# Performance work log

Hardware: AMD Instinct MI355X
Metric: run time of the kernel (lower is better)

## Reference

```python
import jax, jax.numpy as jnp
import numpy as np

HIDDEN = 1024
NUM_HEADS = 16
HEAD_DIM = HIDDEN // NUM_HEADS
SCALE = HEAD_DIM ** -0.5
BATCH = 32
T_CACHED = 2047


def setup_inputs() -> dict:
    key = jax.random.key(0)
    ks = jax.random.split(key, 8)
    hidden_states = jax.random.normal(ks[0], (BATCH, 1, HIDDEN), dtype=jnp.float32)
    key_cache = jax.random.normal(ks[1], (BATCH, NUM_HEADS, T_CACHED, HEAD_DIM), dtype=jnp.float32)
    value_cache = jax.random.normal(ks[2], (BATCH, NUM_HEADS, T_CACHED, HEAD_DIM), dtype=jnp.float32)
    block_tables = jax.random.randint(ks[3], (BATCH, 128), 0, 1024, dtype=jnp.int64 if jax.config.jax_enable_x64 else jnp.int32)
    # valid lengths in [1, T_cached+1]
    seq_lens = jax.random.randint(ks[4], (BATCH,), 1, T_CACHED + 2, dtype=jnp.int32)
    W_attn = jax.random.normal(ks[5], (HIDDEN, 3 * HIDDEN), dtype=jnp.float32) * (HIDDEN ** -0.5)
    b_attn = jnp.zeros((3 * HIDDEN,), dtype=jnp.float32)
    W_proj = jax.random.normal(ks[6], (HIDDEN, HIDDEN), dtype=jnp.float32) * (HIDDEN ** -0.5)
    b_proj = jnp.zeros((HIDDEN,), dtype=jnp.float32)
    return {
        "hidden_states": hidden_states,
        "key_cache": key_cache,
        "value_cache": value_cache,
        "block_tables": block_tables,
        "seq_lens": seq_lens,
        "max_seq_len": T_CACHED + 1,
        "W_attn": W_attn,
        "b_attn": b_attn,
        "W_proj": W_proj,
        "b_proj": b_proj,
    }


def reference(hidden_states, key_cache, value_cache, block_tables, seq_lens,
              max_seq_len, W_attn, b_attn, W_proj, b_proj):
    B, S, H = hidden_states.shape  # S == 1 (single-query decode)
    hs = hidden_states.reshape(B, H)
    qkv = hs @ W_attn + b_attn                      # [B, 3H]
    q, k, v = jnp.split(qkv, 3, axis=-1)
    q = q.reshape(B, NUM_HEADS, HEAD_DIM)           # [B, h, d]
    k = k.reshape(B, NUM_HEADS, 1, HEAD_DIM)
    v = v.reshape(B, NUM_HEADS, 1, HEAD_DIM)
    K = jnp.concatenate([key_cache, k], axis=2)     # [B, h, T, d]
    V = jnp.concatenate([value_cache, v], axis=2)
    T = K.shape[2]
    # single-query attention: scores [B, h, T]
    scores = jnp.einsum('bhd,bhtd->bht', q, K) * SCALE
    pos = jnp.arange(T)
    # attend to first seq_len cached tokens; the freshly appended token (pos T-1) is always visible
    valid = (pos[None, :] < seq_lens[:, None]) | (pos[None, :] == T - 1)  # [B, T]
    scores = jnp.where(valid[:, None, :], scores, jnp.float32(-1e30))
    p = jax.nn.softmax(scores, axis=-1)
    out = jnp.einsum('bht,bhtd->bhd', p, V)         # [B, h, d]
    attn_output = out.reshape(B, S, H) @ W_proj + b_proj
    return attn_output, K, V
```

## Files before the change

### kernel.cpp

```cpp
#include <hip/hip_runtime.h>
#include <math.h>

#define BATCH   32
#define NH      16
#define HD      64
#define T_ALL   2048
#define T_CACHE 2047
#define HID     1024
#define H3      3072
#define QK_SCALE 0.125f
#define NCHUNK  16
#define CHTOK   128
#define NWIN    8
#define KSPLIT  8

typedef float f4 __attribute__((ext_vector_type(4)));

template<int NB>
__global__ __launch_bounds__(256) void gemv_part_kernel(
    const float* __restrict__ X, const float* __restrict__ W,
    float* __restrict__ part, int N, int Kdim)
{
    const int c  = blockIdx.x * 256 + threadIdx.x;
    const int ks = blockIdx.y;
    const int b0 = blockIdx.z * NB;
    const int kchunk = Kdim / KSPLIT;
    float acc[NB];
#pragma unroll
    for (int j = 0; j < NB; ++j) acc[j] = 0.f;
    const int k0 = ks * kchunk;
#pragma unroll 16
    for (int k = k0; k < k0 + kchunk; ++k) {
        const float w = W[(size_t)k * N + c];
#pragma unroll
        for (int j = 0; j < NB; ++j)
            acc[j] = fmaf(X[(b0 + j) * Kdim + k], w, acc[j]);
    }
#pragma unroll
    for (int j = 0; j < NB; ++j)
        part[((size_t)ks * BATCH + b0 + j) * N + c] = acc[j];
}

__global__ __launch_bounds__(256) void gemv_reduce_kernel(
    const float* __restrict__ part, const float* __restrict__ bias,
    float* __restrict__ out, int N)
{
    const int c4 = blockIdx.x * 256 + threadIdx.x;
    const int b  = blockIdx.y;
    const int N4 = N >> 2;
    f4 acc = ((const f4*)bias)[c4];
#pragma unroll
    for (int ks = 0; ks < KSPLIT; ++ks) {
        const f4 p = ((const f4*)part)[((size_t)ks * BATCH + b) * N4 + c4];
        acc.x += p.x; acc.y += p.y; acc.z += p.z; acc.w += p.w;
    }
    ((f4*)out)[(size_t)b * N4 + c4] = acc;
}

__global__ __launch_bounds__(256, 4) void fused_copy_attn_kernel(
    const float* __restrict__ kc, const float* __restrict__ vc,
    const float* __restrict__ qkv, const int* __restrict__ seq_lens,
    float* __restrict__ Kout, float* __restrict__ Vout,
    float* __restrict__ Pm, float* __restrict__ Pl, float* __restrict__ Po)
{
    const int chunk = blockIdx.x;
    const int h     = blockIdx.y;
    const int b     = blockIdx.z;
    const int tid   = threadIdx.x;
    const int wave  = tid >> 6;
    const int lane  = tid & 63;
    const int dgrp  = lane & 15;
    const int tgrp  = lane >> 4;

    const int bh   = b * NH + h;
    const int slen = seq_lens[b];

    const f4 q4 = ((const f4*)(qkv + (size_t)b * H3 + h * HD))[dgrp];

    const int t0 = chunk * CHTOK + wave * (NWIN * 4);
    const int tl = t0 + tgrp;
    const int nat  = min(NWIN, max(0, (slen - t0 + 3) >> 2));
    const bool tail = (t0 + NWIN * 4 - 1 >= T_CACHE);

    const f4* kbase = (const f4*)(kc + (size_t)bh * T_CACHE * HD) + (size_t)tl * 16 + dgrp;
    const f4* vbase = (const f4*)(vc + (size_t)bh * T_CACHE * HD) + (size_t)tl * 16 + dgrp;
    f4* Kb = (f4*)(Kout + (size_t)bh * T_ALL * HD) + (size_t)tl * 16 + dgrp;
    f4* Vb = (f4*)(Vout + (size_t)bh * T_ALL * HD) + (size_t)tl * 16 + dgrp;

    f4 kreg[NWIN], vreg[NWIN];
    float s[NWIN];

    if (!tail) {
#pragma unroll
        for (int i = 0; i < NWIN; ++i)
            kreg[i] = __builtin_nontemporal_load(kbase + i * 64);
#pragma unroll
        for (int i = 0; i < NWIN; ++i)
            vreg[i] = __builtin_nontemporal_load(vbase + i * 64);

#pragma unroll
        for (int i = 0; i < NWIN; ++i) {
            __builtin_nontemporal_store(kreg[i], Kb + i * 64);
            if (i < nat) {
                const f4 kv = kreg[i];
                float ss = kv.x * q4.x + kv.y * q4.y + kv.z * q4.z + kv.w * q4.w;
                ss += __shfl_xor(ss, 1);
                ss += __shfl_xor(ss, 2);
                ss += __shfl_xor(ss, 4);
                ss += __shfl_xor(ss, 8);
                s[i] = (tl + i * 4 < slen) ? ss * QK_SCALE : -1e30f;
            }
        }
    } else {
#pragma unroll
        for (int i = 0; i < NWIN; ++i) {
            const int t = tl + i * 4;
            kreg[i] = (f4){0.f, 0.f, 0.f, 0.f};
            vreg[i] = (f4){0.f, 0.f, 0.f, 0.f};
            if (t < T_CACHE) {
                kreg[i] = __builtin_nontemporal_load(kbase + i * 64);
                vreg[i] = __builtin_nontemporal_load(vbase + i * 64);
            }
        }
#pragma unroll
        for (int i = 0; i < NWIN; ++i) {
            const int t = tl + i * 4;
            if (t < T_CACHE)
                __builtin_nontemporal_store(kreg[i], Kb + i * 64);
            if (i < nat) {
                const f4 kv = kreg[i];
                float ss = kv.x * q4.x + kv.y * q4.y + kv.z * q4.z + kv.w * q4.w;
                ss += __shfl_xor(ss, 1);
                ss += __shfl_xor(ss, 2);
                ss += __shfl_xor(ss, 4);
                ss += __shfl_xor(ss, 8);
                s[i] = (t < slen && t < T_CACHE) ? ss * QK_SCALE : -1e30f;
            }
        }
    }

    float m = -1e30f;
#pragma unroll
    for (int i = 0; i < NWIN; ++i)
        if (i < nat) m = fmaxf(m, s[i]);
    m = fmaxf(m, __shfl_xor(m, 16));
    m = fmaxf(m, __shfl_xor(m, 32));

    float l = 0.f;
#pragma unroll
    for (int i = 0; i < NWIN; ++i)
        if (i < nat) {
            const float p = __expf(s[i] - m);
            s[i] = p;
            l += p;
        }

    f4 o = {0.f, 0.f, 0.f, 0.f};
    if (!tail) {
#pragma unroll
        for (int i = 0; i < NWIN; ++i) {
            __builtin_nontemporal_store(vreg[i], Vb + i * 64);
            if (i < nat) {
                o.x = fmaf(s[i], vreg[i].x, o.x);
                o.y = fmaf(s[i], vreg[i].y, o.y);
                o.z = fmaf(s[i], vreg[i].z, o.z);
                o.w = fmaf(s[i], vreg[i].w, o.w);
            }
        }
    } else {
#pragma unroll
        for (int i = 0; i < NWIN; ++i) {
            const int t = tl + i * 4;
            if (t < T_CACHE)
                __builtin_nontemporal_store(vreg[i], Vb + i * 64);
            if (i < nat) {
                o.x = fmaf(s[i], vreg[i].x, o.x);
                o.y = fmaf(s[i], vreg[i].y, o.y);
                o.z = fmaf(s[i], vreg[i].z, o.z);
                o.w = fmaf(s[i], vreg[i].w, o.w);
            }
        }
    }

    l += __shfl_xor(l, 16); l += __shfl_xor(l, 32);
    o.x += __shfl_xor(o.x, 16); o.x += __shfl_xor(o.x, 32);
    o.y += __shfl_xor(o.y, 16); o.y += __shfl_xor(o.y, 32);
    o.z += __shfl_xor(o.z, 16); o.z += __shfl_xor(o.z, 32);
    o.w += __shfl_xor(o.w, 16); o.w += __shfl_xor(o.w, 32);

    __shared__ float sm[4], sl[4];
    __shared__ f4 so4[4][16];
    if (lane == 0) { sm[wave] = m; sl[wave] = l; }
    if (lane < 16) so4[wave][dgrp] = o;
    __syncthreads();

    if (tid < HD) {
        const int d = tid;
        const float m0 = sm[0], m1 = sm[1], m2 = sm[2], m3 = sm[3];
        const float mc = fmaxf(fmaxf(m0, m1), fmaxf(m2, m3));
        const float e0 = __expf(m0 - mc), e1 = __expf(m1 - mc);
        const float e2 = __expf(m2 - mc), e3 = __expf(m3 - mc);
        const float lc = sl[0]*e0 + sl[1]*e1 + sl[2]*e2 + sl[3]*e3;
        const float* so = (const float*)so4;
        const float oc = so[0*HD + d]*e0 + so[1*HD + d]*e1
                       + so[2*HD + d]*e2 + so[3*HD + d]*e3;
        const int pb = bh * NCHUNK + chunk;
        Po[(size_t)pb * HD + d] = oc;
        if (d == 0) { Pm[pb] = mc; Pl[pb] = lc; }
    }
}

__global__ __launch_bounds__(64) void combine_kernel(
    const float* __restrict__ qkv,
    const float* __restrict__ Pm, const float* __restrict__ Pl,
    const float* __restrict__ Po,
    float* __restrict__ attn, float* __restrict__ Kout, float* __restrict__ Vout)
{
    const int bh = blockIdx.x;
    const int b = bh >> 4, h = bh & 15;
    const int d = threadIdx.x;

    const float* qb = qkv + (size_t)b * H3;
    const float qd = qb[h * HD + d];
    const float kn = qb[HID  + h * HD + d];
    const float vn = qb[2*HID + h * HD + d];

    Kout[((size_t)bh * T_ALL + (T_ALL - 1)) * HD + d] = kn;
    Vout[((size_t)bh * T_ALL + (T_ALL - 1)) * HD + d] = vn;

    float s = qd * kn;
    s += __shfl_xor(s, 1);
    s += __shfl_xor(s, 2);
    s += __shfl_xor(s, 4);
    s += __shfl_xor(s, 8);
    s += __shfl_xor(s, 16);
    s += __shfl_xor(s, 32);
    s *= QK_SCALE;

    float mg = s;
#pragma unroll
    for (int c = 0; c < NCHUNK; ++c)
        mg = fmaxf(mg, Pm[bh * NCHUNK + c]);

    float L   = __expf(s - mg);
    float acc = L * vn;
#pragma unroll
    for (int c = 0; c < NCHUNK; ++c) {
        const float e = __expf(Pm[bh * NCHUNK + c] - mg);
        acc += Po[(size_t)(bh * NCHUNK + c) * HD + d] * e;
        L   += Pl[bh * NCHUNK + c] * e;
    }
    attn[(size_t)b * HID + h * HD + d] = acc / L;
}

extern "C" void kernel_launch(void* const* d_in, const int* in_sizes, int n_in,
                              void* d_out, int out_size, void* d_ws, size_t ws_size,
                              hipStream_t stream)
{
    const float* hs       = (const float*)d_in[0];
    const float* kc       = (const float*)d_in[1];
    const float* vc       = (const float*)d_in[2];
    const int*   seq_lens = (const int*)d_in[4];
    const float* W_attn   = (const float*)d_in[6];
    const float* b_attn   = (const float*)d_in[7];
    const float* W_proj   = (const float*)d_in[8];
    const float* b_proj   = (const float*)d_in[9];

    float* out_attn = (float*)d_out;
    float* Kout = out_attn + (size_t)BATCH * HID;
    float* Vout = Kout + (size_t)BATCH * NH * T_ALL * HD;

    float* w = (float*)d_ws;
    float* w_qkv_part  = w;
    float* w_qkv       = w_qkv_part + (size_t)KSPLIT * BATCH * H3;
    float* w_Pm        = w_qkv + (size_t)BATCH * H3;
    float* w_Pl        = w_Pm + BATCH * NH * NCHUNK;
    float* w_Po        = w_Pl + BATCH * NH * NCHUNK;
    float* w_attnvec   = w_Po + (size_t)BATCH * NH * NCHUNK * HD;
    float* w_proj_part = w_attnvec + (size_t)BATCH * HID;

    gemv_part_kernel<16><<<dim3(H3 / 256, KSPLIT, 2), 256, 0, stream>>>(
        hs, W_attn, w_qkv_part, H3, HID);
    gemv_reduce_kernel<<<dim3(H3 / 4 / 256, BATCH), 256, 0, stream>>>(
        w_qkv_part, b_attn, w_qkv, H3);

    fused_copy_attn_kernel<<<dim3(NCHUNK, NH, BATCH), 256, 0, stream>>>(
        kc, vc, w_qkv, seq_lens, Kout, Vout, w_Pm, w_Pl, w_Po);

    combine_kernel<<<dim3(BATCH * NH), 64, 0, stream>>>(
        w_qkv, w_Pm, w_Pl, w_Po, w_attnvec, Kout, Vout);

    gemv_part_kernel<8><<<dim3(HID / 256, KSPLIT, 4), 256, 0, stream>>>(
        w_attnvec, W_proj, w_proj_part, HID, HID);
    gemv_reduce_kernel<<<dim3(HID / 4 / 256, BATCH), 256, 0, stream>>>(
        w_proj_part, b_proj, out_attn, HID);
}
```

Measured before the change: 251.3 us.

## Fuse QKV split-K reduction into attention and combine; halve chunk size

Removes the separate QKV reduce kernel launch. The attention and combine kernels now sum the split-K partials plus bias themselves, which costs a few redundant loads per block. It also doubles the number of attention chunks (64 tokens each, 4 windows per wave) and raises the occupancy hint to 6 blocks per CU, aiming for more parallelism and lower register pressure. The trade-off is a larger combine step and more partial-result traffic.

```diff
diff --git a/kernel.cpp b/kernel.cpp
--- a/kernel.cpp
+++ b/kernel.cpp
@@ -9,9 +9,9 @@
 #define HID     1024
 #define H3      3072
 #define QK_SCALE 0.125f
-#define NCHUNK  16
-#define CHTOK   128
-#define NWIN    8
+#define NCHUNK  32
+#define CHTOK   64
+#define NWIN    4
 #define KSPLIT  8
 
 typedef float f4 __attribute__((ext_vector_type(4)));
@@ -57,9 +57,10 @@
     ((f4*)out)[(size_t)b * N4 + c4] = acc;
 }
 
-__global__ __launch_bounds__(256, 4) void fused_copy_attn_kernel(
+__global__ __launch_bounds__(256, 6) void fused_copy_attn_kernel(
     const float* __restrict__ kc, const float* __restrict__ vc,
-    const float* __restrict__ qkv, const int* __restrict__ seq_lens,
+    const float* __restrict__ qkv_part, const float* __restrict__ b_attn,
+    const int* __restrict__ seq_lens,
     float* __restrict__ Kout, float* __restrict__ Vout,
     float* __restrict__ Pm, float* __restrict__ Pl, float* __restrict__ Po)
 {
@@ -75,7 +76,12 @@
     const int bh   = b * NH + h;
     const int slen = seq_lens[b];
 
-    const f4 q4 = ((const f4*)(qkv + (size_t)b * H3 + h * HD))[dgrp];
+    f4 q4 = ((const f4*)(b_attn + h * HD))[dgrp];
+#pragma unroll
+    for (int ks = 0; ks < KSPLIT; ++ks) {
+        const f4 p = ((const f4*)(qkv_part + ((size_t)ks * BATCH + b) * H3 + h * HD))[dgrp];
+        q4.x += p.x; q4.y += p.y; q4.z += p.z; q4.w += p.w;
+    }
 
     const int t0 = chunk * CHTOK + wave * (NWIN * 4);
     const int tl = t0 + tgrp;
@@ -211,7 +217,7 @@
 }
 
 __global__ __launch_bounds__(64) void combine_kernel(
-    const float* __restrict__ qkv,
+    const float* __restrict__ qkv_part, const float* __restrict__ b_attn,
     const float* __restrict__ Pm, const float* __restrict__ Pl,
     const float* __restrict__ Po,
     float* __restrict__ attn, float* __restrict__ Kout, float* __restrict__ Vout)
@@ -220,10 +226,16 @@
     const int b = bh >> 4, h = bh & 15;
     const int d = threadIdx.x;
 
-    const float* qb = qkv + (size_t)b * H3;
-    const float qd = qb[h * HD + d];
-    const float kn = qb[HID  + h * HD + d];
-    const float vn = qb[2*HID + h * HD + d];
+    float qd = b_attn[h * HD + d];
+    float kn = b_attn[HID  + h * HD + d];
+    float vn = b_attn[2*HID + h * HD + d];
+#pragma unroll
+    for (int ks = 0; ks < KSPLIT; ++ks) {
+        const float* pp = qkv_part + ((size_t)ks * BATCH + b) * H3;
+        qd += pp[h * HD + d];
+        kn += pp[HID  + h * HD + d];
+        vn += pp[2*HID + h * HD + d];
+    }
 
     Kout[((size_t)bh * T_ALL + (T_ALL - 1)) * HD + d] = kn;
     Vout[((size_t)bh * T_ALL + (T_ALL - 1)) * HD + d] = vn;
@@ -238,13 +250,13 @@
     s *= QK_SCALE;
 
     float mg = s;
-#pragma unroll
+#pragma unroll 16
     for (int c = 0; c < NCHUNK; ++c)
         mg = fmaxf(mg, Pm[bh * NCHUNK + c]);
 
     float L   = __expf(s - mg);
     float acc = L * vn;
-#pragma unroll
+#pragma unroll 8
     for (int c = 0; c < NCHUNK; ++c) {
         const float e = __expf(Pm[bh * NCHUNK + c] - mg);
         acc += Po[(size_t)(bh * NCHUNK + c) * HD + d] * e;
@@ -272,8 +284,7 @@
 
     float* w = (float*)d_ws;
     float* w_qkv_part  = w;
-    float* w_qkv       = w_qkv_part + (size_t)KSPLIT * BATCH * H3;
-    float* w_Pm        = w_qkv + (size_t)BATCH * H3;
+    float* w_Pm        = w_qkv_part + (size_t)KSPLIT * BATCH * H3;
     float* w_Pl        = w_Pm + BATCH * NH * NCHUNK;
     float* w_Po        = w_Pl + BATCH * NH * NCHUNK;
     float* w_attnvec   = w_Po + (size_t)BATCH * NH * NCHUNK * HD;
@@ -281,14 +292,12 @@
 
     gemv_part_kernel<16><<<dim3(H3 / 256, KSPLIT, 2), 256, 0, stream>>>(
         hs, W_attn, w_qkv_part, H3, HID);
-    gemv_reduce_kernel<<<dim3(H3 / 4 / 256, BATCH), 256, 0, stream>>>(
-        w_qkv_part, b_attn, w_qkv, H3);
 
     fused_copy_attn_kernel<<<dim3(NCHUNK, NH, BATCH), 256, 0, stream>>>(
-        kc, vc, w_qkv, seq_lens, Kout, Vout, w_Pm, w_Pl, w_Po);
+        kc, vc, w_qkv_part, b_attn, seq_lens, Kout, Vout, w_Pm, w_Pl, w_Po);
 
     combine_kernel<<<dim3(BATCH * NH), 64, 0, stream>>>(
-        w_qkv, w_Pm, w_Pl, w_Po, w_attnvec, Kout, Vout);
+        w_qkv_part, b_attn, w_Pm, w_Pl, w_Po, w_attnvec, Kout, Vout);
 
     gemv_part_kernel<8><<<dim3(HID / 256, KSPLIT, 4), 256, 0, stream>>>(
         w_attnvec, W_proj, w_proj_part, HID, HID);
```

New measurement: 243.0 us (median of 2 runs). 1.03x faster.

## Split fused K/V copy-attention into separate K-score and V-accumulate kernels

Applied to the files above, without the earlier changes.

The single kernel that copied K and V while computing chunked attention becomes two kernels. The first copies K, computes scores and the chunk-max-normalised probabilities, and writes them to workspace. The second copies V and accumulates the probability-weighted output. The aim is to halve register pressure per kernel (occupancy hint raised from 4 to 6) so more loads are in flight, at the cost of an extra launch and a round trip of the probabilities through global memory. The workspace is also reorganised so several scratch buffers share one region.

```diff
diff --git a/kernel.cpp b/kernel.cpp
--- a/kernel.cpp
+++ b/kernel.cpp
@@ -57,11 +57,11 @@
     ((f4*)out)[(size_t)b * N4 + c4] = acc;
 }
 
-__global__ __launch_bounds__(256, 4) void fused_copy_attn_kernel(
-    const float* __restrict__ kc, const float* __restrict__ vc,
-    const float* __restrict__ qkv, const int* __restrict__ seq_lens,
-    float* __restrict__ Kout, float* __restrict__ Vout,
-    float* __restrict__ Pm, float* __restrict__ Pl, float* __restrict__ Po)
+__global__ __launch_bounds__(256, 6) void k_copy_score_kernel(
+    const float* __restrict__ kc, const float* __restrict__ qkv,
+    const int* __restrict__ seq_lens,
+    float* __restrict__ Kout,
+    float* __restrict__ Pm, float* __restrict__ Pl, float* __restrict__ P)
 {
     const int chunk = blockIdx.x;
     const int h     = blockIdx.y;
@@ -73,21 +73,19 @@
     const int tgrp  = lane >> 4;
 
     const int bh   = b * NH + h;
-    const int slen = seq_lens[b];
+    const int vlim = min(seq_lens[b], T_CACHE);
 
     const f4 q4 = ((const f4*)(qkv + (size_t)b * H3 + h * HD))[dgrp];
 
     const int t0 = chunk * CHTOK + wave * (NWIN * 4);
     const int tl = t0 + tgrp;
-    const int nat  = min(NWIN, max(0, (slen - t0 + 3) >> 2));
+    const int nat  = min(NWIN, max(0, (vlim - t0 + 3) >> 2));
     const bool tail = (t0 + NWIN * 4 - 1 >= T_CACHE);
 
     const f4* kbase = (const f4*)(kc + (size_t)bh * T_CACHE * HD) + (size_t)tl * 16 + dgrp;
-    const f4* vbase = (const f4*)(vc + (size_t)bh * T_CACHE * HD) + (size_t)tl * 16 + dgrp;
     f4* Kb = (f4*)(Kout + (size_t)bh * T_ALL * HD) + (size_t)tl * 16 + dgrp;
-    f4* Vb = (f4*)(Vout + (size_t)bh * T_ALL * HD) + (size_t)tl * 16 + dgrp;
-
-    f4 kreg[NWIN], vreg[NWIN];
+
+    f4 kreg[NWIN];
     float s[NWIN];
 
     if (!tail) {
@@ -95,47 +93,38 @@
         for (int i = 0; i < NWIN; ++i)
             kreg[i] = __builtin_nontemporal_load(kbase + i * 64);
 #pragma unroll
-        for (int i = 0; i < NWIN; ++i)
-            vreg[i] = __builtin_nontemporal_load(vbase + i * 64);
-
-#pragma unroll
         for (int i = 0; i < NWIN; ++i) {
             __builtin_nontemporal_store(kreg[i], Kb + i * 64);
-            if (i < nat) {
-                const f4 kv = kreg[i];
-                float ss = kv.x * q4.x + kv.y * q4.y + kv.z * q4.z + kv.w * q4.w;
-                ss += __shfl_xor(ss, 1);
-                ss += __shfl_xor(ss, 2);
-                ss += __shfl_xor(ss, 4);
-                ss += __shfl_xor(ss, 8);
-                s[i] = (tl + i * 4 < slen) ? ss * QK_SCALE : -1e30f;
-            }
+            s[i] = kreg[i].x * q4.x + kreg[i].y * q4.y
+                 + kreg[i].z * q4.z + kreg[i].w * q4.w;
         }
     } else {
 #pragma unroll
         for (int i = 0; i < NWIN; ++i) {
             const int t = tl + i * 4;
             kreg[i] = (f4){0.f, 0.f, 0.f, 0.f};
-            vreg[i] = (f4){0.f, 0.f, 0.f, 0.f};
-            if (t < T_CACHE) {
+            if (t < T_CACHE)
                 kreg[i] = __builtin_nontemporal_load(kbase + i * 64);
-                vreg[i] = __builtin_nontemporal_load(vbase + i * 64);
-            }
         }
 #pragma unroll
         for (int i = 0; i < NWIN; ++i) {
             const int t = tl + i * 4;
             if (t < T_CACHE)
                 __builtin_nontemporal_store(kreg[i], Kb + i * 64);
-            if (i < nat) {
-                const f4 kv = kreg[i];
-                float ss = kv.x * q4.x + kv.y * q4.y + kv.z * q4.z + kv.w * q4.w;
-                ss += __shfl_xor(ss, 1);
-                ss += __shfl_xor(ss, 2);
-                ss += __shfl_xor(ss, 4);
-                ss += __shfl_xor(ss, 8);
-                s[i] = (t < slen && t < T_CACHE) ? ss * QK_SCALE : -1e30f;
-            }
+            s[i] = kreg[i].x * q4.x + kreg[i].y * q4.y
+                 + kreg[i].z * q4.z + kreg[i].w * q4.w;
+        }
+    }
+
+#pragma unroll
+    for (int i = 0; i < NWIN; ++i) {
+        if (i < nat) {
+            float ss = s[i];
+            ss += __shfl_xor(ss, 1);
+            ss += __shfl_xor(ss, 2);
+            ss += __shfl_xor(ss, 4);
+            ss += __shfl_xor(ss, 8);
+            s[i] = (tl + i * 4 < vlim) ? ss * QK_SCALE : -1e30f;
         }
     }
 
@@ -146,26 +135,95 @@
     m = fmaxf(m, __shfl_xor(m, 16));
     m = fmaxf(m, __shfl_xor(m, 32));
 
+    __shared__ float sm[4], sl[4];
+    if (lane == 0) sm[wave] = m;
+    __syncthreads();
+    const float mc = fmaxf(fmaxf(sm[0], sm[1]), fmaxf(sm[2], sm[3]));
+
     float l = 0.f;
 #pragma unroll
     for (int i = 0; i < NWIN; ++i)
         if (i < nat) {
-            const float p = __expf(s[i] - m);
+            const float p = __expf(s[i] - mc);
             s[i] = p;
             l += p;
         }
+    l += __shfl_xor(l, 16); l += __shfl_xor(l, 32);
+
+    const int pb = bh * NCHUNK + chunk;
+    if (dgrp == 0) {
+#pragma unroll
+        for (int i = 0; i < NWIN; ++i)
+            if (i < nat)
+                P[(size_t)pb * CHTOK + wave * (NWIN * 4) + i * 4 + tgrp] = s[i];
+    }
+    if (lane == 0) sl[wave] = l;
+    __syncthreads();
+    if (tid == 0) {
+        Pm[pb] = mc;
+        Pl[pb] = sl[0] + sl[1] + sl[2] + sl[3];
+    }
+}
+
+__global__ __launch_bounds__(256, 6) void v_copy_accum_kernel(
+    const float* __restrict__ vc, const int* __restrict__ seq_lens,
+    const float* __restrict__ P,
+    float* __restrict__ Vout, float* __restrict__ Po)
+{
+    const int chunk = blockIdx.x;
+    const int h     = blockIdx.y;
+    const int b     = blockIdx.z;
+    const int tid   = threadIdx.x;
+    const int wave  = tid >> 6;
+    const int lane  = tid & 63;
+    const int dgrp  = lane & 15;
+    const int tgrp  = lane >> 4;
+
+    const int bh   = b * NH + h;
+    const int vlim = min(seq_lens[b], T_CACHE);
+
+    const int t0 = chunk * CHTOK + wave * (NWIN * 4);
+    const int tl = t0 + tgrp;
+    const int nat  = min(NWIN, max(0, (vlim - t0 + 3) >> 2));
+    const bool tail = (t0 + NWIN * 4 - 1 >= T_CACHE);
+
+    const f4* vbase = (const f4*)(vc + (size_t)bh * T_CACHE * HD) + (size_t)tl * 16 + dgrp;
+    f4* Vb = (f4*)(Vout + (size_t)bh * T_ALL * HD) + (size_t)tl * 16 + dgrp;
+
+    const int pb = bh * NCHUNK + chunk;
+
+    float pw[NWIN];
+#pragma unroll
+    for (int i = 0; i < NWIN; ++i) {
+        pw[i] = 0.f;
+        if (i < nat)
+            pw[i] = P[(size_t)pb * CHTOK + wave * (NWIN * 4) + i * 4 + tgrp];
+    }
+
+    f4 vreg[NWIN];
+    if (!tail) {
+#pragma unroll
+        for (int i = 0; i < NWIN; ++i)
+            vreg[i] = __builtin_nontemporal_load(vbase + i * 64);
+    } else {
+#pragma unroll
+        for (int i = 0; i < NWIN; ++i) {
+            const int t = tl + i * 4;
+            vreg[i] = (f4){0.f, 0.f, 0.f, 0.f};
+            if (t < T_CACHE)
+                vreg[i] = __builtin_nontemporal_load(vbase + i * 64);
+        }
+    }
 
     f4 o = {0.f, 0.f, 0.f, 0.f};
     if (!tail) {
 #pragma unroll
         for (int i = 0; i < NWIN; ++i) {
             __builtin_nontemporal_store(vreg[i], Vb + i * 64);
-            if (i < nat) {
-                o.x = fmaf(s[i], vreg[i].x, o.x);
-                o.y = fmaf(s[i], vreg[i].y, o.y);
-                o.z = fmaf(s[i], vreg[i].z, o.z);
-                o.w = fmaf(s[i], vreg[i].w, o.w);
-            }
+            o.x = fmaf(pw[i], vreg[i].x, o.x);
+            o.y = fmaf(pw[i], vreg[i].y, o.y);
+            o.z = fmaf(pw[i], vreg[i].z, o.z);
+            o.w = fmaf(pw[i], vreg[i].w, o.w);
         }
     } else {
 #pragma unroll
@@ -173,40 +231,28 @@
             const int t = tl + i * 4;
             if (t < T_CACHE)
                 __builtin_nontemporal_store(vreg[i], Vb + i * 64);
-            if (i < nat) {
-                o.x = fmaf(s[i], vreg[i].x, o.x);
-                o.y = fmaf(s[i], vreg[i].y, o.y);
-                o.z = fmaf(s[i], vreg[i].z, o.z);
-                o.w = fmaf(s[i], vreg[i].w, o.w);
-            }
-        }
-    }
-
-    l += __shfl_xor(l, 16); l += __shfl_xor(l, 32);
+            o.x = fmaf(pw[i], vreg[i].x, o.x);
+            o.y = fmaf(pw[i], vreg[i].y, o.y);
+            o.z = fmaf(pw[i], vreg[i].z, o.z);
+            o.w = fmaf(pw[i], vreg[i].w, o.w);
+        }
+    }
+
     o.x += __shfl_xor(o.x, 16); o.x += __shfl_xor(o.x, 32);
     o.y += __shfl_xor(o.y, 16); o.y += __shfl_xor(o.y, 32);
     o.z += __shfl_xor(o.z, 16); o.z += __shfl_xor(o.z, 32);
     o.w += __shfl_xor(o.w, 16); o.w += __shfl_xor(o.w, 32);
 
-    __shared__ float sm[4], sl[4];
     __shared__ f4 so4[4][16];
-    if (lane == 0) { sm[wave] = m; sl[wave] = l; }
     if (lane < 16) so4[wave][dgrp] = o;
     __syncthreads();
 
     if (tid < HD) {
         const int d = tid;
-        const float m0 = sm[0], m1 = sm[1], m2 = sm[2], m3 = sm[3];
-        const float mc = fmaxf(fmaxf(m0, m1), fmaxf(m2, m3));
-        const float e0 = __expf(m0 - mc), e1 = __expf(m1 - mc);
-        const float e2 = __expf(m2 - mc), e3 = __expf(m3 - mc);
-        const float lc = sl[0]*e0 + sl[1]*e1 + sl[2]*e2 + sl[3]*e3;
         const float* so = (const float*)so4;
-        const float oc = so[0*HD + d]*e0 + so[1*HD + d]*e1
-                       + so[2*HD + d]*e2 + so[3*HD + d]*e3;
-        const int pb = bh * NCHUNK + chunk;
+        const float oc = so[0*HD + d] + so[1*HD + d]
+                       + so[2*HD + d] + so[3*HD + d];
         Po[(size_t)pb * HD + d] = oc;
-        if (d == 0) { Pm[pb] = mc; Pl[pb] = lc; }
     }
 }
 
@@ -244,7 +290,7 @@
 
     float L   = __expf(s - mg);
     float acc = L * vn;
-#pragma unroll
+#pragma unroll 8
     for (int c = 0; c < NCHUNK; ++c) {
         const float e = __expf(Pm[bh * NCHUNK + c] - mg);
         acc += Po[(size_t)(bh * NCHUNK + c) * HD + d] * e;
@@ -271,21 +317,26 @@
     float* Vout = Kout + (size_t)BATCH * NH * T_ALL * HD;
 
     float* w = (float*)d_ws;
-    float* w_qkv_part  = w;
-    float* w_qkv       = w_qkv_part + (size_t)KSPLIT * BATCH * H3;
+    float* w_union     = w;
+    float* w_qkv_part  = w_union;
+    float* w_P         = w_union;
+    float* w_proj_part = w_union;
+    float* w_qkv       = w + 1048576;
     float* w_Pm        = w_qkv + (size_t)BATCH * H3;
     float* w_Pl        = w_Pm + BATCH * NH * NCHUNK;
     float* w_Po        = w_Pl + BATCH * NH * NCHUNK;
     float* w_attnvec   = w_Po + (size_t)BATCH * NH * NCHUNK * HD;
-    float* w_proj_part = w_attnvec + (size_t)BATCH * HID;
 
     gemv_part_kernel<16><<<dim3(H3 / 256, KSPLIT, 2), 256, 0, stream>>>(
         hs, W_attn, w_qkv_part, H3, HID);
     gemv_reduce_kernel<<<dim3(H3 / 4 / 256, BATCH), 256, 0, stream>>>(
         w_qkv_part, b_attn, w_qkv, H3);
 
-    fused_copy_attn_kernel<<<dim3(NCHUNK, NH, BATCH), 256, 0, stream>>>(
-        kc, vc, w_qkv, seq_lens, Kout, Vout, w_Pm, w_Pl, w_Po);
+    k_copy_score_kernel<<<dim3(NCHUNK, NH, BATCH), 256, 0, stream>>>(
+        kc, w_qkv, seq_lens, Kout, w_Pm, w_Pl, w_P);
+
+    v_copy_accum_kernel<<<dim3(NCHUNK, NH, BATCH), 256, 0, stream>>>(
+        vc, seq_lens, w_P, Vout, w_Po);
 
     combine_kernel<<<dim3(BATCH * NH), 64, 0, stream>>>(
         w_qkv, w_Pm, w_Pl, w_Po, w_attnvec, Kout, Vout);
```

Result: no change. 248.2 us (-1.2%).
